# Performance work log

Measured on AMD Instinct MI355X. Metric: run time of the kernel, lower is better.

The kernel has to match this reference:

```python
import jax, jax.numpy as jnp
import numpy as np

B, S, D_MODEL, N_HEADS, MAX_LEN = 2, 1024, 1024, 16, 1024
D_K = D_MODEL // N_HEADS


def setup_inputs() -> dict:
    key = jax.random.key(0)
    ks = jax.random.split(key, 8)
    w_std = 1.0 / np.sqrt(D_MODEL)  # ~ torch Linear default scale
    inp = {
        "query": jax.random.normal(ks[0], (B, S, D_MODEL), jnp.float32),
        "key": jax.random.normal(ks[1], (B, S, D_MODEL), jnp.float32),
        "value": jax.random.normal(ks[2], (B, S, D_MODEL), jnp.float32),
        "Wq": jax.random.normal(ks[3], (D_MODEL, D_MODEL), jnp.float32) * w_std,
        "Wk": jax.random.normal(ks[4], (D_MODEL, D_MODEL), jnp.float32) * w_std,
        "Wv": jax.random.normal(ks[5], (D_MODEL, D_MODEL), jnp.float32) * w_std,
        "Wo": jax.random.normal(ks[6], (D_MODEL, D_MODEL), jnp.float32) * w_std,
        "bq": jnp.zeros((D_MODEL,), jnp.float32),
        "bk": jnp.zeros((D_MODEL,), jnp.float32),
        "bv": jnp.zeros((D_MODEL,), jnp.float32),
        "bo": jnp.zeros((D_MODEL,), jnp.float32),
        "Er": jax.random.normal(ks[7], (2 * MAX_LEN - 1, D_K), jnp.float32) * 0.02,
    }
    return inp


def _rel_positions(q_len, k_len, max_len):
    pos = jnp.arange(q_len)[:, None] - jnp.arange(k_len)[None, :]
    pos = jnp.clip(pos, -max_len + 1, max_len - 1)
    return pos + max_len - 1  # [q_len, k_len] indices into Er


def reference(query, key, value, Wq, Wk, Wv, Wo, bq, bk, bv, bo, Er):
    b, q_len, d_model = query.shape
    k_len = key.shape[1]
    d_k = Er.shape[-1]
    h = d_model // d_k
    scale = 1.0 / np.sqrt(d_k)

    def proj(x, W, bias):  # torch Linear: x @ W.T + b, then split heads -> [b,h,s,d_k]
        y = x @ W.T + bias
        return y.reshape(b, -1, h, d_k).transpose(0, 2, 1, 3)

    q = proj(query, Wq, bq)
    k = proj(key, Wk, bk)
    v = proj(value, Wv, bv)

    positions = _rel_positions(q_len, k_len, MAX_LEN)  # [q,k]
    # QEr[b,h,q,k] = sum_d q[b,h,q,d] * Er[positions[q,k], d]
    # computed as a full contraction against Er then a gather on the relative axis
    qe_all = jnp.einsum('bhqd,rd->bhqr', q, Er)  # [b,h,q,2*max_len-1]
    qer = jnp.take_along_axis(qe_all, positions[None, None, :, :], axis=-1)  # [b,h,q,k]

    qk = jnp.einsum('bhqd,bhkd->bhqk', q, k)
    scores = (qk + qer) * scale
    p_attn = jax.nn.softmax(scores, axis=-1)  # dropout=0.0 (eval)
    out = jnp.einsum('bhqk,bhkd->bhqd', p_attn, v)

    out = out.transpose(0, 2, 1, 3).reshape(b, q_len, h * d_k)
    return out @ Wo.T + bo
```

## Files before the change

### kernel.cpp

```cpp
#include <hip/hip_runtime.h>
#include <hip/hip_bf16.h>
#include <cstdint>
#include <cstddef>

typedef __attribute__((ext_vector_type(8))) short bf16x8;
typedef __attribute__((ext_vector_type(4))) float f32x4;
typedef unsigned short u16;
typedef unsigned int u32;

#define DEV static __device__ __forceinline__

constexpr int Sc = 1024, DMc = 1024, Hc = 16, DKc = 64;

DEV u16 f2bf(float f) {
  u32 u = __float_as_uint(f);
  return (u16)((u + 0x7FFFu + ((u >> 16) & 1u)) >> 16);
}
DEV float bf2f(u16 h) { return __uint_as_float(((u32)h) << 16); }

#define GLDS16(g, l)                                                        \
  __builtin_amdgcn_global_load_lds(                                         \
      (const __attribute__((address_space(1))) void*)(g),                   \
      (__attribute__((address_space(3))) void*)(l), 16, 0, 0)

struct CvtJob { const float* in; u16* out; int nchunk; int rsh; int nreal; };
struct CvtArgs { CvtJob j[8]; };

__global__ __launch_bounds__(256) void cvt_kernel(CvtArgs a) {
  CvtJob job = a.j[blockIdx.y];
  int ci = (int)(blockIdx.x * 256 + threadIdx.x);
  if (ci >= job.nchunk) return;
  bf16x8 o = {};
  if (ci < job.nreal) {
    const float* src = job.in + (size_t)ci * 8;
    float4 v0 = *(const float4*)src;
    float4 v1 = *(const float4*)(src + 4);
    o[0] = (short)f2bf(v0.x); o[1] = (short)f2bf(v0.y);
    o[2] = (short)f2bf(v0.z); o[3] = (short)f2bf(v0.w);
    o[4] = (short)f2bf(v1.x); o[5] = (short)f2bf(v1.y);
    o[6] = (short)f2bf(v1.z); o[7] = (short)f2bf(v1.w);
  }
  int row = ci >> job.rsh;
  int co = (ci & ~7) | ((ci & 7) ^ (row & 7));
  *(bf16x8*)(job.out + (size_t)co * 8) = o;
}

struct GemmJob { const u16* A; const u16* W; const float* bias; void* out; };
struct GemmArgs { GemmJob p[3]; };

template<int BM, int BN, int MODE>
__global__ __launch_bounds__(256, 2) void gemm_bt(GemmArgs G) {
  constexpr int MI = BM / 32, NI = BN / 32;
  __shared__ __align__(16) u16 sA[2][BM * 64];
  __shared__ __align__(16) u16 sB[2][BN * 64];
  const int tid = threadIdx.x, lane = tid & 63, w = tid >> 6;
  const int cl = lane & 15, rg = lane >> 4;
  const int srow = lane >> 3, schk = lane & 7;
  int z, m0, n0;
  if (MODE == 0) {
    int id = blockIdx.x;
    if (id < 512) {
      z = id >> 8;
      int r = id & 255, xcd = r & 7, t = r >> 3;
      m0 = (xcd * 4 + (t & 3)) * 64;
      n0 = (t >> 2) * 128;
    } else {
      z = 2;
      int r = id - 512, xcd = r & 7, t = r >> 3;
      n0 = (xcd * 2 + (t & 1)) * 128;
      m0 = (t >> 1) * 64;
    }
  } else {
    z = 0;
    int id = blockIdx.x, xcd = id & 7, t = id >> 3;
    m0 = (xcd * 4 + (t & 3)) * 64;
    n0 = (t >> 2) * 64;
  }
  GemmJob P = G.p[z];
  constexpr int K = 1024;
  const int wm = (w >> 1) * (BM / 2), wn = (w & 1) * (BN / 2);
  f32x4 acc[MI][NI] = {};

  auto stage = [&](int kt, int b) {
    const u16* Ab = P.A + (size_t)m0 * K + kt * 64;
    const u16* Wb = P.W + (size_t)n0 * K + kt * 64;
    #pragma unroll
    for (int i = 0; i < BM / 32; ++i)
      GLDS16(Ab + (size_t)(i * 32 + w * 8 + srow) * K + schk * 8, &sA[b][(i * 32 + w * 8) * 64]);
    #pragma unroll
    for (int i = 0; i < BN / 32; ++i)
      GLDS16(Wb + (size_t)(i * 32 + w * 8 + srow) * K + schk * 8, &sB[b][(i * 32 + w * 8) * 64]);
  };

  stage(0, 0);
  for (int kt = 0; kt < 16; ++kt) {
    __syncthreads();
    if (kt < 15) stage(kt + 1, (kt + 1) & 1);
    const u16* A_ = sA[kt & 1];
    const u16* B_ = sB[kt & 1];
    #pragma unroll
    for (int kk = 0; kk < 2; ++kk) {
      bf16x8 af[MI], bfr[NI];
      #pragma unroll
      for (int mi = 0; mi < MI; ++mi) {
        int row = wm + mi * 16 + cl;
        af[mi] = *(const bf16x8*)(A_ + row * 64 + ((kk * 4 + rg) ^ (row & 7)) * 8);
      }
      #pragma unroll
      for (int ni = 0; ni < NI; ++ni) {
        int row = wn + ni * 16 + cl;
        bfr[ni] = *(const bf16x8*)(B_ + row * 64 + ((kk * 4 + rg) ^ (row & 7)) * 8);
      }
      #pragma unroll
      for (int mi = 0; mi < MI; ++mi)
        #pragma unroll
        for (int ni = 0; ni < NI; ++ni)
          acc[mi][ni] = __builtin_amdgcn_mfma_f32_16x16x32_bf16(af[mi], bfr[ni], acc[mi][ni], 0, 0, 0);
    }
  }
  #pragma unroll
  for (int mi = 0; mi < MI; ++mi) {
    #pragma unroll
    for (int ni = 0; ni < NI; ++ni) {
      #pragma unroll
      for (int j = 0; j < 4; ++j) {
        int m = m0 + wm + mi * 16 + rg * 4 + j;
        int n = n0 + wn + ni * 16 + cl;
        if (MODE == 1) {
          ((float*)P.out)[(size_t)m * DMc + n] = acc[mi][ni][j] + P.bias[n];
        } else if (z < 2) {
          float v = acc[mi][ni][j] + P.bias[n];
          int h = n >> 6, d = n & 63;
          int c2 = (d >> 3) ^ (m & 7);
          ((u16*)P.out)[((size_t)((m >> 10) * Hc + h) * Sc + (m & 1023)) * DKc + c2 * 8 + (d & 7)] = f2bf(v);
        } else {
          float v = acc[mi][ni][j] + P.bias[m];
          int d = m & 63, h = m >> 6, bb = n >> 10, s = n & 1023;
          int c2 = ((s & 63) >> 3) ^ (d & 7);
          ((u16*)P.out)[((size_t)(bb * Hc + h) * DKc + d) * Sc + (s & ~63) + c2 * 8 + (s & 7)] = f2bf(v);
        }
      }
    }
  }
}

__global__ __launch_bounds__(256, 4) void attn_rel(
    const u16* __restrict__ qg, const u16* __restrict__ kg,
    const u16* __restrict__ vtg, const u16* __restrict__ erg,
    u16* __restrict__ Opart, float* __restrict__ lpart) {
  __shared__ __align__(16) u16 sK[64 * 64];
  __shared__ __align__(16) u16 sV[64 * 64];
  __shared__ __align__(16) u16 sU[4][1440];
  const int tid = threadIdx.x, lane = tid & 63, w = tid >> 6;
  const int cl = lane & 15, rg = lane >> 4;
  const int key = cl & 7;
  const int bh = blockIdx.x & 31, qt = (blockIdx.x >> 5) & 15, half = blockIdx.x >> 9;
  const int q0 = qt * 64, t0 = half * 8;

  const u16* qrow = qg + ((size_t)bh * Sc + q0 + w * 16 + cl) * DKc;
  bf16x8 qf0 = *(const bf16x8*)(qrow + (rg ^ key) * 8);
  bf16x8 qf1 = *(const bf16x8*)(qrow + ((rg + 4) ^ key) * 8);
  f32x4 oacc[4] = {};
  float lsum = 0.f;
  u16* Uw = sU[w];
  const u16* kbase = kg + (size_t)bh * Sc * DKc;
  const u16* vbase = vtg + (size_t)bh * DKc * Sc;

  auto stage = [&](int t) {
    const u16* ks = kbase + t * 64 * 64;
    #pragma unroll
    for (int i = 0; i < 2; ++i) {
      GLDS16(ks + (i * 32 + w * 8) * 64 + lane * 8, &sK[(i * 32 + w * 8) * 64]);
      GLDS16(vbase + (size_t)(i * 32 + w * 8 + (lane >> 3)) * Sc + t * 64 + (lane & 7) * 8,
             &sV[(i * 32 + w * 8) * 64]);
    }
  };

  stage(t0);
  for (int tt = 0; tt < 8; ++tt) {
    const int t = t0 + tt;
    __syncthreads();

    f32x4 sct[4];
    #pragma unroll
    for (int nc = 0; nc < 4; ++nc) {
      const u16* kr = sK + (nc * 16 + cl) * 64;
      bf16x8 b0 = *(const bf16x8*)(kr + (rg ^ key) * 8);
      bf16x8 b1 = *(const bf16x8*)(kr + ((rg + 4) ^ key) * 8);
      f32x4 a = {};
      a = __builtin_amdgcn_mfma_f32_16x16x32_bf16(b0, qf0, a, 0, 0, 0);
      a = __builtin_amdgcn_mfma_f32_16x16x32_bf16(b1, qf1, a, 0, 0, 0);
      sct[nc] = a;
    }
    const u16* ebase = erg + (size_t)(q0 + w * 16 - t * 64 + 960) * DKc;
    #pragma unroll
    for (int rc0 = 0; rc0 < 5; ++rc0) {
      const u16* er = ebase + (size_t)(rc0 * 16 + cl) * DKc;
      bf16x8 e0 = *(const bf16x8*)(er + (rg ^ key) * 8);
      bf16x8 e1 = *(const bf16x8*)(er + ((rg + 4) ^ key) * 8);
      f32x4 a = {};
      a = __builtin_amdgcn_mfma_f32_16x16x32_bf16(qf0, e0, a, 0, 0, 0);
      a = __builtin_amdgcn_mfma_f32_16x16x32_bf16(qf1, e1, a, 0, 0, 0);
      u16* tp = Uw + (rc0 * 16 + cl) * 18 + rg * 4;
      ushort2 lo, hi;
      lo.x = f2bf(a[0]); lo.y = f2bf(a[1]);
      hi.x = f2bf(a[2]); hi.y = f2bf(a[3]);
      *(ushort2*)tp = lo;
      *(ushort2*)(tp + 2) = hi;
    }
    float pv[4][4];
    #pragma unroll
    for (int nc = 0; nc < 4; ++nc) {
      #pragma unroll
      for (int j = 0; j < 4; ++j) {
        int r = cl + 63 - (nc * 16 + rg * 4 + j);
        float tval = bf2f(Uw[r * 18 + cl]);
        float p = __expf((sct[nc][j] + tval) * 0.125f);
        lsum += p;
        pv[nc][j] = p;
      }
    }
    #pragma unroll
    for (int nc = 0; nc < 4; ++nc) {
      ushort4 pk;
      pk.x = f2bf(pv[nc][0]); pk.y = f2bf(pv[nc][1]);
      pk.z = f2bf(pv[nc][2]); pk.w = f2bf(pv[nc][3]);
      *(ushort4*)(Uw + cl * 76 + nc * 16 + rg * 4) = pk;
    }
    bf16x8 pa0 = *(const bf16x8*)(Uw + cl * 76 + rg * 8);
    bf16x8 pa1 = *(const bf16x8*)(Uw + cl * 76 + 32 + rg * 8);
    #pragma unroll
    for (int dc = 0; dc < 4; ++dc) {
      const u16* vr = sV + (dc * 16 + cl) * 64;
      bf16x8 b0 = *(const bf16x8*)(vr + (rg ^ key) * 8);
      bf16x8 b1 = *(const bf16x8*)(vr + ((rg + 4) ^ key) * 8);
      oacc[dc] = __builtin_amdgcn_mfma_f32_16x16x32_bf16(pa0, b0, oacc[dc], 0, 0, 0);
      oacc[dc] = __builtin_amdgcn_mfma_f32_16x16x32_bf16(pa1, b1, oacc[dc], 0, 0, 0);
    }
    __syncthreads();
    if (tt < 7) stage(t + 1);
  }
  lsum += __shfl_xor(lsum, 16);
  lsum += __shfl_xor(lsum, 32);
  const size_t pb = (size_t)(half * 32 + bh) * Sc;
  if (rg == 0) lpart[pb + q0 + w * 16 + cl] = lsum;
  u16* Ob = Opart + (pb + q0 + w * 16) * DKc;
  #pragma unroll
  for (int dc = 0; dc < 4; ++dc)
    #pragma unroll
    for (int j = 0; j < 4; ++j)
      Ob[(rg * 4 + j) * DKc + dc * 16 + cl] = f2bf(oacc[dc][j]);
}

__global__ __launch_bounds__(256) void merge_kernel(
    const u16* __restrict__ O, const float* __restrict__ l,
    u16* __restrict__ attnb) {
  int ci = (int)(blockIdx.x * 256 + threadIdx.x);
  int bh = ci >> 13, rem = ci & 8191, s = rem >> 3, dc = rem & 7;
  const u16* o0 = O + ((size_t)bh * Sc + s) * DKc + dc * 8;
  const u16* o1 = o0 + (size_t)32 * Sc * DKc;
  float rinv = 1.0f / (l[(size_t)bh * Sc + s] + l[(size_t)(32 + bh) * Sc + s]);
  bf16x8 a = *(const bf16x8*)o0;
  bf16x8 b = *(const bf16x8*)o1;
  bf16x8 o;
  #pragma unroll
  for (int e = 0; e < 8; ++e)
    o[e] = (short)f2bf((bf2f((u16)a[e]) + bf2f((u16)b[e])) * rinv);
  int bb = bh >> 4, h = bh & 15;
  int c2 = dc ^ (s & 7);
  *(bf16x8*)(attnb + ((size_t)(bb * Sc + s)) * DMc + h * DKc + c2 * 8) = o;
}

extern "C" void kernel_launch(void* const* d_in, const int* in_sizes, int n_in,
                              void* d_out, int out_size, void* d_ws, size_t ws_size,
                              hipStream_t stream) {
  (void)in_sizes; (void)n_in; (void)out_size; (void)ws_size;
  const float* query = (const float*)d_in[0];
  const float* key_  = (const float*)d_in[1];
  const float* value = (const float*)d_in[2];
  const float* Wq = (const float*)d_in[3];
  const float* Wk = (const float*)d_in[4];
  const float* Wv = (const float*)d_in[5];
  const float* Wo = (const float*)d_in[6];
  const float* bq = (const float*)d_in[7];
  const float* bk = (const float*)d_in[8];
  const float* bv = (const float*)d_in[9];
  const float* bo = (const float*)d_in[10];
  const float* Er = (const float*)d_in[11];

  char* p = (char*)d_ws;
  size_t off = 0;
  auto alloc = [&](size_t bytes) {
    char* r = p + off;
    off += (bytes + 255) & ~(size_t)255;
    return r;
  };
  u16* Xq  = (u16*)alloc((size_t)2048 * 1024 * 2);
  u16* Xk  = (u16*)alloc((size_t)2048 * 1024 * 2);
  u16* Xv  = (u16*)alloc((size_t)2048 * 1024 * 2);
  u16* Wqb = (u16*)alloc((size_t)1024 * 1024 * 2);
  u16* Wkb = (u16*)alloc((size_t)1024 * 1024 * 2);
  u16* Wvb = (u16*)alloc((size_t)1024 * 1024 * 2);
  u16* Wob = (u16*)alloc((size_t)1024 * 1024 * 2);
  u16* Erb = (u16*)alloc((size_t)2048 * 64 * 2);
  u16* qh  = (u16*)alloc((size_t)2048 * 1024 * 2);
  u16* kh  = (u16*)alloc((size_t)2048 * 1024 * 2);
  u16* vt  = (u16*)alloc((size_t)2048 * 1024 * 2);
  u16* attnb = (u16*)alloc((size_t)2048 * 1024 * 2);
  u16* Opart = (u16*)alloc((size_t)2 * 32 * 1024 * 64 * 2);
  float* lpart = (float*)alloc((size_t)2 * 32 * 1024 * 4);

  CvtArgs ca;
  ca.j[0] = {query, Xq, 262144, 7, 262144};
  ca.j[1] = {key_,  Xk, 262144, 7, 262144};
  ca.j[2] = {value, Xv, 262144, 7, 262144};
  ca.j[3] = {Wq, Wqb, 131072, 7, 131072};
  ca.j[4] = {Wk, Wkb, 131072, 7, 131072};
  ca.j[5] = {Wv, Wvb, 131072, 7, 131072};
  ca.j[6] = {Wo, Wob, 131072, 7, 131072};
  ca.j[7] = {Er, Erb, 16384, 3, 16376};
  cvt_kernel<<<dim3(1024, 8, 1), 256, 0, stream>>>(ca);

  GemmArgs gp;
  gp.p[0] = {Xq, Wqb, bq, (void*)qh};
  gp.p[1] = {Xk, Wkb, bk, (void*)kh};
  gp.p[2] = {Wvb, Xv, bv, (void*)vt};
  gemm_bt<64, 128, 0><<<dim3(768, 1, 1), 256, 0, stream>>>(gp);

  attn_rel<<<dim3(1024, 1, 1), 256, 0, stream>>>(qh, kh, vt, Erb, Opart, lpart);

  merge_kernel<<<dim3(1024, 1, 1), 256, 0, stream>>>(Opart, lpart, attnb);

  GemmArgs go;
  go.p[0] = {attnb, Wob, bo, d_out};
  go.p[1] = go.p[0];
  go.p[2] = go.p[0];
  gemm_bt<64, 64, 1><<<dim3(512, 1, 1), 256, 0, stream>>>(go);
}
```

Baseline: 91.64 us.

## Fuse split-K attention merge into output projection GEMM A-tile loads

Result: no change. 92.54 us (+1.0%).

```diff
diff --git a/kernel.cpp b/kernel.cpp
--- a/kernel.cpp
+++ b/kernel.cpp
@@ -45,7 +45,7 @@
   *(bf16x8*)(job.out + (size_t)co * 8) = o;
 }
 
-struct GemmJob { const u16* A; const u16* W; const float* bias; void* out; };
+struct GemmJob { const u16* A; const u16* W; const float* bias; void* out; const float* aux; };
 struct GemmArgs { GemmJob p[3]; };
 
 template<int BM, int BN, int MODE>
@@ -81,23 +81,54 @@
   const int wm = (w >> 1) * (BM / 2), wn = (w & 1) * (BN / 2);
   f32x4 acc[MI][NI] = {};
 
+  bf16x8 ma[2][2];
+  float  ml[2][2];
+
   auto stage = [&](int kt, int b) {
-    const u16* Ab = P.A + (size_t)m0 * K + kt * 64;
+    if (MODE == 0) {
+      const u16* Ab = P.A + (size_t)m0 * K + kt * 64;
+      #pragma unroll
+      for (int i = 0; i < BM / 32; ++i)
+        GLDS16(Ab + (size_t)(i * 32 + w * 8 + srow) * K + schk * 8, &sA[b][(i * 32 + w * 8) * 64]);
+    } else {
+      #pragma unroll
+      for (int i = 0; i < 2; ++i) {
+        int ch = i * 256 + tid, row = ch >> 3, c = ch & 7;
+        int rgl = m0 + row, bb = rgl >> 10, s = rgl & 1023;
+        const u16* o0 = P.A + ((size_t)(bb * 16 + kt) * 1024 + s) * 64 + c * 8;
+        ma[i][0] = *(const bf16x8*)o0;
+        ma[i][1] = *(const bf16x8*)(o0 + (size_t)32 * 1024 * 64);
+        ml[i][0] = P.aux[(size_t)(bb * 16 + kt) * 1024 + s];
+        ml[i][1] = P.aux[(size_t)(32 + bb * 16 + kt) * 1024 + s];
+      }
+    }
     const u16* Wb = P.W + (size_t)n0 * K + kt * 64;
-    #pragma unroll
-    for (int i = 0; i < BM / 32; ++i)
-      GLDS16(Ab + (size_t)(i * 32 + w * 8 + srow) * K + schk * 8, &sA[b][(i * 32 + w * 8) * 64]);
     #pragma unroll
     for (int i = 0; i < BN / 32; ++i)
       GLDS16(Wb + (size_t)(i * 32 + w * 8 + srow) * K + schk * 8, &sB[b][(i * 32 + w * 8) * 64]);
   };
 
+  auto commit = [&](int b) {
+    #pragma unroll
+    for (int i = 0; i < 2; ++i) {
+      int ch = i * 256 + tid, row = ch >> 3, c = ch & 7;
+      float rinv = 1.0f / (ml[i][0] + ml[i][1]);
+      bf16x8 v8;
+      #pragma unroll
+      for (int e = 0; e < 8; ++e)
+        v8[e] = (short)f2bf((bf2f((u16)ma[i][0][e]) + bf2f((u16)ma[i][1][e])) * rinv);
+      *(bf16x8*)(sA[b] + row * 64 + (c ^ (row & 7)) * 8) = v8;
+    }
+  };
+
   stage(0, 0);
+  if (MODE == 1) commit(0);
   for (int kt = 0; kt < 16; ++kt) {
     __syncthreads();
-    if (kt < 15) stage(kt + 1, (kt + 1) & 1);
-    const u16* A_ = sA[kt & 1];
-    const u16* B_ = sB[kt & 1];
+    const int b = kt & 1;
+    if (kt < 15) stage(kt + 1, b ^ 1);
+    const u16* A_ = sA[b];
+    const u16* B_ = sB[b];
     #pragma unroll
     for (int kk = 0; kk < 2; ++kk) {
       bf16x8 af[MI], bfr[NI];
@@ -117,6 +148,7 @@
         for (int ni = 0; ni < NI; ++ni)
           acc[mi][ni] = __builtin_amdgcn_mfma_f32_16x16x32_bf16(af[mi], bfr[ni], acc[mi][ni], 0, 0, 0);
     }
+    if (MODE == 1 && kt < 15) commit(b ^ 1);
   }
   #pragma unroll
   for (int mi = 0; mi < MI; ++mi) {
@@ -250,25 +282,6 @@
     #pragma unroll
     for (int j = 0; j < 4; ++j)
       Ob[(rg * 4 + j) * DKc + dc * 16 + cl] = f2bf(oacc[dc][j]);
-}
-
-__global__ __launch_bounds__(256) void merge_kernel(
-    const u16* __restrict__ O, const float* __restrict__ l,
-    u16* __restrict__ attnb) {
-  int ci = (int)(blockIdx.x * 256 + threadIdx.x);
-  int bh = ci >> 13, rem = ci & 8191, s = rem >> 3, dc = rem & 7;
-  const u16* o0 = O + ((size_t)bh * Sc + s) * DKc + dc * 8;
-  const u16* o1 = o0 + (size_t)32 * Sc * DKc;
-  float rinv = 1.0f / (l[(size_t)bh * Sc + s] + l[(size_t)(32 + bh) * Sc + s]);
-  bf16x8 a = *(const bf16x8*)o0;
-  bf16x8 b = *(const bf16x8*)o1;
-  bf16x8 o;
-  #pragma unroll
-  for (int e = 0; e < 8; ++e)
-    o[e] = (short)f2bf((bf2f((u16)a[e]) + bf2f((u16)b[e])) * rinv);
-  int bb = bh >> 4, h = bh & 15;
-  int c2 = dc ^ (s & 7);
-  *(bf16x8*)(attnb + ((size_t)(bb * Sc + s)) * DMc + h * DKc + c2 * 8) = o;
 }
 
 extern "C" void kernel_launch(void* const* d_in, const int* in_sizes, int n_in,
@@ -306,7 +319,6 @@
   u16* qh  = (u16*)alloc((size_t)2048 * 1024 * 2);
   u16* kh  = (u16*)alloc((size_t)2048 * 1024 * 2);
   u16* vt  = (u16*)alloc((size_t)2048 * 1024 * 2);
-  u16* attnb = (u16*)alloc((size_t)2048 * 1024 * 2);
   u16* Opart = (u16*)alloc((size_t)2 * 32 * 1024 * 64 * 2);
   float* lpart = (float*)alloc((size_t)2 * 32 * 1024 * 4);
 
@@ -322,17 +334,15 @@
   cvt_kernel<<<dim3(1024, 8, 1), 256, 0, stream>>>(ca);
 
   GemmArgs gp;
-  gp.p[0] = {Xq, Wqb, bq, (void*)qh};
-  gp.p[1] = {Xk, Wkb, bk, (void*)kh};
-  gp.p[2] = {Wvb, Xv, bv, (void*)vt};
+  gp.p[0] = {Xq, Wqb, bq, (void*)qh, nullptr};
+  gp.p[1] = {Xk, Wkb, bk, (void*)kh, nullptr};
+  gp.p[2] = {Wvb, Xv, bv, (void*)vt, nullptr};
   gemm_bt<64, 128, 0><<<dim3(768, 1, 1), 256, 0, stream>>>(gp);
 
   attn_rel<<<dim3(1024, 1, 1), 256, 0, stream>>>(qh, kh, vt, Erb, Opart, lpart);
 
-  merge_kernel<<<dim3(1024, 1, 1), 256, 0, stream>>>(Opart, lpart, attnb);
-
   GemmArgs go;
-  go.p[0] = {attnb, Wob, bo, d_out};
+  go.p[0] = {Opart, Wob, bo, d_out, lpart};
   go.p[1] = go.p[0];
   go.p[2] = go.p[0];
   gemm_bt<64, 64, 1><<<dim3(512, 1, 1), 256, 0, stream>>>(go);
```
